# Kernel tuning notes

Measured on AMD Instinct MI355X. Metric: run time of the kernel, lower is better.

The kernel has to match this reference:

```python
import jax, jax.numpy as jnp
import numpy as np
from jax import lax

N_INPUTS = 8
N_OUTPUTS = 4
N_RESERVOIR = 2048
T = 4096
SPECTRAL_RADIUS = 0.95
NOISE = 0.001


def setup_inputs() -> dict:
    key = jax.random.key(0)
    ks = jax.random.split(key, 8)
    inputs = jax.random.normal(ks[0], (T, N_INPUTS), dtype=jnp.float32)
    outputs = jax.random.normal(ks[1], (T, N_OUTPUTS), dtype=jnp.float32)
    # recurrent weights: uniform(-0.5, 0.5), rescaled to spectral radius ~0.95.
    # For a uniform(-0.5,0.5) NxN matrix the spectral radius is ~ sqrt(N/12)
    # (circular law), used here in place of an explicit eigendecomposition.
    w_raw = jax.random.uniform(ks[2], (N_RESERVOIR, N_RESERVOIR), dtype=jnp.float32) - 0.5
    radius = jnp.sqrt(N_RESERVOIR / 12.0)
    w = w_raw * (SPECTRAL_RADIUS / radius)
    w_in = jax.random.uniform(ks[3], (N_RESERVOIR, N_INPUTS), dtype=jnp.float32) * 2.0 - 1.0
    w_feedb = jax.random.uniform(ks[4], (N_RESERVOIR, N_OUTPUTS), dtype=jnp.float32) * 2.0 - 1.0
    # readout (nn.Linear): weight [n_out, R+n_in], bias [n_out]
    fan_in = N_RESERVOIR + N_INPUTS
    bound = 1.0 / np.sqrt(fan_in)
    lin_w = jax.random.uniform(ks[5], (N_OUTPUTS, fan_in), dtype=jnp.float32, minval=-bound, maxval=bound)
    lin_b = jax.random.uniform(ks[6], (N_OUTPUTS,), dtype=jnp.float32, minval=-bound, maxval=bound)
    # per-step regularization noise: noise * (uniform - 0.5), pre-drawn for determinism
    noise_seq = NOISE * (jax.random.uniform(ks[7], (T, N_RESERVOIR), dtype=jnp.float32) - 0.5)
    return {"inputs": inputs, "outputs": outputs, "w": w, "w_in": w_in,
            "w_feedb": w_feedb, "lin_w": lin_w, "lin_b": lin_b, "noise_seq": noise_seq}


def reference(inputs, outputs, w, w_in, w_feedb, lin_w, lin_b, noise_seq):
    # Echo-state recurrence: x_n = tanh(w @ x_{n-1} + w_in @ u_n + w_feedb @ y_{n-1}) + noise_n
    # States row 0 stays zero (original loop starts at n=1).
    R = w.shape[0]

    def step(x, per_step):
        u_n, y_prev, nz = per_step
        x_new = jnp.tanh(w @ x + w_in @ u_n + w_feedb @ y_prev) + nz
        return x_new, x_new

    x0 = jnp.zeros((R,), dtype=inputs.dtype)
    _, xs = lax.scan(step, x0, (inputs[1:], outputs[:-1], noise_seq[1:]))  # [T-1, R]

    zero_row_x = jnp.zeros((1, R), dtype=inputs.dtype)
    zero_row_u = jnp.zeros((1, inputs.shape[1]), dtype=inputs.dtype)
    states_x = jnp.concatenate([zero_row_x, xs], axis=0)              # [T, R]
    states_u = jnp.concatenate([zero_row_u, inputs[1:]], axis=0)       # [T, n_in]
    states = jnp.concatenate([states_x, states_u], axis=1)             # [T, R+n_in]

    out = states @ lin_w.T + lin_b                                     # [T, n_out]
    return out
```

## Files before the change

### kernel.cpp

```cpp
#include <hip/hip_runtime.h>

#define T_STEPS 4096
#define RSIZE   2048
#define N_IN    8
#define N_OUT   4
#define NWG     256
#define NT      256
#define LIN_STRIDE  (RSIZE + N_IN)
#define SENTINEL    0x7FC00000u

typedef float v4 __attribute__((ext_vector_type(4)));


__global__ __launch_bounds__(256) void init_kernel(v4* __restrict__ states4) {
    int idx = blockIdx.x * 256 + threadIdx.x;
    const float s = __uint_as_float(SENTINEL);
    v4 v = (idx < RSIZE / 4) ? (v4){0.f, 0.f, 0.f, 0.f} : (v4){s, s, s, s};
    states4[idx] = v;
}

__device__ __forceinline__ float dot4(v4 a, v4 b) {
    float s = a.x * b.x;
    s = fmaf(a.y, b.y, s);
    s = fmaf(a.z, b.z, s);
    s = fmaf(a.w, b.w, s);
    return s;
}

__global__ __launch_bounds__(NT, 1) void reservoir_kernel(
    const float* __restrict__ W,
    const float* __restrict__ Win,
    const float* __restrict__ Wfb,
    const float* __restrict__ inputs,
    const float* __restrict__ outputs,
    const float* __restrict__ noise,
    float* __restrict__ states)
{
    const int g    = blockIdx.x;
    const int t    = threadIdx.x;
    const int lane = t & 63;
    const int wv   = t >> 6;
    const int wid  = g * 4 + wv;
    const int r0   = wid * 2;

    v4 wreg[2][4][2];
    #pragma unroll
    for (int i = 0; i < 2; ++i)
        #pragma unroll
        for (int j = 0; j < 4; ++j) {
            const float* p = W + (size_t)(r0 + i) * RSIZE + j * 512 + lane * 8;
            wreg[i][j][0] = *(const v4*)p;
            wreg[i][j][1] = *(const v4*)(p + 4);
        }

    float win[N_IN] = {0}, wfb[N_OUT] = {0};
    if (lane < 2) {
        const int r = r0 + lane;
        #pragma unroll
        for (int j = 0; j < N_IN; ++j)  win[j] = Win[r * N_IN + j];
        #pragma unroll
        for (int k = 0; k < N_OUT; ++k) wfb[k] = Wfb[r * N_OUT + k];
    }

    __shared__ v4 xsh[2][RSIZE / 4];
    const int fillc = wv * 512 + lane * 8;
    const int fi    = fillc >> 2;

    for (int n = 1; n < T_STEPS; ++n) {
        float pre = 0.0f, nz = 0.0f;
        if (lane < 2) {
            const int r = r0 + lane;
            nz = noise[(size_t)n * RSIZE + r];
            #pragma unroll
            for (int j = 0; j < N_IN; ++j)  pre = fmaf(win[j], inputs[n * N_IN + j], pre);
            #pragma unroll
            for (int k = 0; k < N_OUT; ++k) pre = fmaf(wfb[k], outputs[(n - 1) * N_OUT + k], pre);
        }

        const volatile v4* src =
            (const volatile v4*)(states + (size_t)(n - 1) * RSIZE + fillc);
        v4 a, b;
        for (;;) {
            a = src[0];
            b = src[1];
            bool ok = (__float_as_uint(a.x) != SENTINEL) &
                      (__float_as_uint(a.y) != SENTINEL) &
                      (__float_as_uint(a.z) != SENTINEL) &
                      (__float_as_uint(a.w) != SENTINEL) &
                      (__float_as_uint(b.x) != SENTINEL) &
                      (__float_as_uint(b.y) != SENTINEL) &
                      (__float_as_uint(b.z) != SENTINEL) &
                      (__float_as_uint(b.w) != SENTINEL);
            if (ok) break;
            __builtin_amdgcn_s_sleep(1);
        }

        const int p = (n - 1) & 1;
        xsh[p][fi]     = a;
        xsh[p][fi + 1] = b;
        __syncthreads();

        float acc0 = 0.0f, acc1 = 0.0f;
        #pragma unroll
        for (int j = 0; j < 4; ++j) {
            const int xi = j * 128 + lane * 2;
            v4 x0 = xsh[p][xi];
            v4 x1 = xsh[p][xi + 1];
            acc0 += dot4(wreg[0][j][0], x0) + dot4(wreg[0][j][1], x1);
            acc1 += dot4(wreg[1][j][0], x0) + dot4(wreg[1][j][1], x1);
        }

        #pragma unroll
        for (int m = 1; m < 64; m <<= 1) {
            acc0 += __shfl_xor(acc0, m, 64);
            acc1 += __shfl_xor(acc1, m, 64);
        }

        if (lane < 2) {
            float s  = (lane == 0 ? acc0 : acc1) + pre;
            float xn = tanhf(s) + nz;
            *(volatile float*)(states + (size_t)n * RSIZE + r0 + lane) = xn;
        }
        __builtin_amdgcn_s_waitcnt(0);
    }
}

__global__ __launch_bounds__(256) void readout_kernel(
    const float* __restrict__ states,
    const float* __restrict__ inputs,
    const float* __restrict__ lin_w,
    const float* __restrict__ lin_b,
    float* __restrict__ out)
{
    const int ti   = blockIdx.x;
    const int tid  = threadIdx.x;
    const int lane = tid & 63;
    const int wave = tid >> 6;
    const int c0   = tid * 8;

    const float* xp = states + (size_t)ti * RSIZE + c0;
    v4 xa = *(const v4*)xp;
    v4 xb = *(const v4*)(xp + 4);

    float acc[N_OUT];
    #pragma unroll
    for (int o = 0; o < N_OUT; ++o) {
        const float* lp = lin_w + (size_t)o * LIN_STRIDE + c0;
        v4 la = *(const v4*)lp;
        v4 lb = *(const v4*)(lp + 4);
        acc[o] = dot4(la, xa) + dot4(lb, xb);
    }

    #pragma unroll
    for (int m = 1; m < 64; m <<= 1) {
        #pragma unroll
        for (int o = 0; o < N_OUT; ++o) acc[o] += __shfl_xor(acc[o], m, 64);
    }

    __shared__ float red[4][N_OUT];
    if (lane == 0) {
        #pragma unroll
        for (int o = 0; o < N_OUT; ++o) red[wave][o] = acc[o];
    }
    __syncthreads();

    if (tid < N_OUT) {
        float s = red[0][tid] + red[1][tid] + red[2][tid] + red[3][tid] + lin_b[tid];
        if (ti > 0) {
            #pragma unroll
            for (int j = 0; j < N_IN; ++j)
                s = fmaf(lin_w[(size_t)tid * LIN_STRIDE + RSIZE + j],
                         inputs[ti * N_IN + j], s);
        }
        out[ti * N_OUT + tid] = s;
    }
}

extern "C" void kernel_launch(void* const* d_in, const int* in_sizes, int n_in,
                              void* d_out, int out_size, void* d_ws, size_t ws_size,
                              hipStream_t stream) {
    const float* inputs  = (const float*)d_in[0];
    const float* outputs = (const float*)d_in[1];
    const float* W       = (const float*)d_in[2];
    const float* Win     = (const float*)d_in[3];
    const float* Wfb     = (const float*)d_in[4];
    const float* lin_w   = (const float*)d_in[5];
    const float* lin_b   = (const float*)d_in[6];
    const float* noise   = (const float*)d_in[7];
    float* out = (float*)d_out;

    float* states = (float*)d_ws;

    hipLaunchKernelGGL(init_kernel, dim3((T_STEPS * RSIZE / 4) / 256), dim3(256), 0,
                       stream, (v4*)states);
    hipLaunchKernelGGL(reservoir_kernel, dim3(NWG), dim3(NT), 0, stream,
                       W, Win, Wfb, inputs, outputs, noise, states);
    hipLaunchKernelGGL(readout_kernel, dim3(T_STEPS), dim3(256), 0, stream,
                       states, inputs, lin_w, lin_b, out);
}
```

Measured before the change: 7.594 ms.

## Halve workgroups to 128 with four rows per wave and transposed reduction

Each wave now computes four reservoir rows instead of two, so only 128 workgroups take part in the per-step global spin-wait handoff. Weights are held in registers with a coalesced layout of one v4 per lane per chunk. The cross-lane reduction uses a butterfly transpose that sums four accumulators with fewer shuffles. Polling is now wave-uniform through __any. Fewer workgroups cut global synchronization and polling traffic per step, at the cost of more register pressure and more FMA work per wave.

```diff
diff --git a/kernel.cpp b/kernel.cpp
--- a/kernel.cpp
+++ b/kernel.cpp
@@ -4,7 +4,7 @@
 #define RSIZE   2048
 #define N_IN    8
 #define N_OUT   4
-#define NWG     256
+#define NWG     128
 #define NT      256
 #define LIN_STRIDE  (RSIZE + N_IN)
 #define SENTINEL    0x7FC00000u
@@ -41,20 +41,17 @@
     const int lane = t & 63;
     const int wv   = t >> 6;
     const int wid  = g * 4 + wv;
-    const int r0   = wid * 2;
-
-    v4 wreg[2][4][2];
+    const int r0   = wid * 4;
+
+    v4 wreg[4][8];
     #pragma unroll
-    for (int i = 0; i < 2; ++i)
-        #pragma unroll
-        for (int j = 0; j < 4; ++j) {
-            const float* p = W + (size_t)(r0 + i) * RSIZE + j * 512 + lane * 8;
-            wreg[i][j][0] = *(const v4*)p;
-            wreg[i][j][1] = *(const v4*)(p + 4);
-        }
+    for (int i = 0; i < 4; ++i)
+        #pragma unroll
+        for (int c = 0; c < 8; ++c)
+            wreg[i][c] = *(const v4*)(W + (size_t)(r0 + i) * RSIZE + c * 256 + lane * 4);
 
     float win[N_IN] = {0}, wfb[N_OUT] = {0};
-    if (lane < 2) {
+    if (lane < 4) {
         const int r = r0 + lane;
         #pragma unroll
         for (int j = 0; j < N_IN; ++j)  win[j] = Win[r * N_IN + j];
@@ -63,12 +60,12 @@
     }
 
     __shared__ v4 xsh[2][RSIZE / 4];
-    const int fillc = wv * 512 + lane * 8;
-    const int fi    = fillc >> 2;
+    const int fi0 = wv * 128 + lane;
+    const int fi1 = wv * 128 + 64 + lane;
 
     for (int n = 1; n < T_STEPS; ++n) {
         float pre = 0.0f, nz = 0.0f;
-        if (lane < 2) {
+        if (lane < 4) {
             const int r = r0 + lane;
             nz = noise[(size_t)n * RSIZE + r];
             #pragma unroll
@@ -77,48 +74,58 @@
             for (int k = 0; k < N_OUT; ++k) pre = fmaf(wfb[k], outputs[(n - 1) * N_OUT + k], pre);
         }
 
-        const volatile v4* src =
-            (const volatile v4*)(states + (size_t)(n - 1) * RSIZE + fillc);
-        v4 a, b;
+        const volatile v4* src0 =
+            (const volatile v4*)(states + (size_t)(n - 1) * RSIZE) + fi0;
+        const volatile v4* src1 =
+            (const volatile v4*)(states + (size_t)(n - 1) * RSIZE) + fi1;
+        v4 a = {0.f, 0.f, 0.f, 0.f}, b = {0.f, 0.f, 0.f, 0.f};
+        bool done = false;
         for (;;) {
-            a = src[0];
-            b = src[1];
-            bool ok = (__float_as_uint(a.x) != SENTINEL) &
-                      (__float_as_uint(a.y) != SENTINEL) &
-                      (__float_as_uint(a.z) != SENTINEL) &
-                      (__float_as_uint(a.w) != SENTINEL) &
-                      (__float_as_uint(b.x) != SENTINEL) &
-                      (__float_as_uint(b.y) != SENTINEL) &
-                      (__float_as_uint(b.z) != SENTINEL) &
-                      (__float_as_uint(b.w) != SENTINEL);
-            if (ok) break;
+            if (!done) {
+                a = *src0;
+                b = *src1;
+                done = (__float_as_uint(a.x) != SENTINEL) &
+                       (__float_as_uint(a.y) != SENTINEL) &
+                       (__float_as_uint(a.z) != SENTINEL) &
+                       (__float_as_uint(a.w) != SENTINEL) &
+                       (__float_as_uint(b.x) != SENTINEL) &
+                       (__float_as_uint(b.y) != SENTINEL) &
+                       (__float_as_uint(b.z) != SENTINEL) &
+                       (__float_as_uint(b.w) != SENTINEL);
+            }
+            if (!__any(!done)) break;
             __builtin_amdgcn_s_sleep(1);
         }
 
         const int p = (n - 1) & 1;
-        xsh[p][fi]     = a;
-        xsh[p][fi + 1] = b;
+        xsh[p][fi0] = a;
+        xsh[p][fi1] = b;
         __syncthreads();
 
-        float acc0 = 0.0f, acc1 = 0.0f;
-        #pragma unroll
-        for (int j = 0; j < 4; ++j) {
-            const int xi = j * 128 + lane * 2;
-            v4 x0 = xsh[p][xi];
-            v4 x1 = xsh[p][xi + 1];
-            acc0 += dot4(wreg[0][j][0], x0) + dot4(wreg[0][j][1], x1);
-            acc1 += dot4(wreg[1][j][0], x0) + dot4(wreg[1][j][1], x1);
-        }
-
-        #pragma unroll
-        for (int m = 1; m < 64; m <<= 1) {
-            acc0 += __shfl_xor(acc0, m, 64);
-            acc1 += __shfl_xor(acc1, m, 64);
-        }
-
-        if (lane < 2) {
-            float s  = (lane == 0 ? acc0 : acc1) + pre;
-            float xn = tanhf(s) + nz;
+        float acc[4] = {0.f, 0.f, 0.f, 0.f};
+        #pragma unroll
+        for (int c = 0; c < 8; ++c) {
+            v4 x = xsh[p][c * 64 + lane];
+            #pragma unroll
+            for (int i = 0; i < 4; ++i) acc[i] = fmaf(1.0f, dot4(wreg[i][c], x), acc[i]);
+        }
+
+        float a0 = (lane & 1) ? acc[1] : acc[0];
+        float s0 = (lane & 1) ? acc[0] : acc[1];
+        float a1 = (lane & 1) ? acc[3] : acc[2];
+        float s1 = (lane & 1) ? acc[2] : acc[3];
+        a0 += __shfl_xor(s0, 1, 64);
+        a1 += __shfl_xor(s1, 1, 64);
+        float b0 = (lane & 2) ? a1 : a0;
+        float sb = (lane & 2) ? a0 : a1;
+        b0 += __shfl_xor(sb, 2, 64);
+        b0 += __shfl_xor(b0, 4, 64);
+        b0 += __shfl_xor(b0, 8, 64);
+        b0 += __shfl_xor(b0, 16, 64);
+        b0 += __shfl_xor(b0, 32, 64);
+
+        if (lane < 4) {
+            float xn = tanhf(b0 + pre) + nz;
             *(volatile float*)(states + (size_t)n * RSIZE + r0 + lane) = xn;
         }
         __builtin_amdgcn_s_waitcnt(0);
```

After: 8.176 ms. 1.08x slower.

## Prefetch next-step inputs, coalesce state polling, and merge dual-row shuffle reduction

Applied to the files above, without the earlier changes.

Precomputes the input and feedback pre-activation and noise for step n+1 while step n runs, so those global loads leave the critical path. State polling now uses contiguous per-lane v4 loads with a wave-wide __all exit, and the W register layout is changed to match. The two row accumulators are folded into a single butterfly reduction, which roughly halves the shuffle count. The trailing s_waitcnt(0) is removed, which could change when the volatile store becomes visible to other workgroups.

```diff
diff --git a/kernel.cpp b/kernel.cpp
--- a/kernel.cpp
+++ b/kernel.cpp
@@ -43,15 +43,12 @@
     const int wid  = g * 4 + wv;
     const int r0   = wid * 2;
 
-    v4 wreg[2][4][2];
+    v4 wreg[2][8];
     #pragma unroll
     for (int i = 0; i < 2; ++i)
         #pragma unroll
-        for (int j = 0; j < 4; ++j) {
-            const float* p = W + (size_t)(r0 + i) * RSIZE + j * 512 + lane * 8;
-            wreg[i][j][0] = *(const v4*)p;
-            wreg[i][j][1] = *(const v4*)(p + 4);
-        }
+        for (int c = 0; c < 8; ++c)
+            wreg[i][c] = *(const v4*)(W + (size_t)(r0 + i) * RSIZE + c * 256 + lane * 4);
 
     float win[N_IN] = {0}, wfb[N_OUT] = {0};
     if (lane < 2) {
@@ -63,65 +60,101 @@
     }
 
     __shared__ v4 xsh[2][RSIZE / 4];
-    const int fillc = wv * 512 + lane * 8;
-    const int fi    = fillc >> 2;
+    const int fi0 = wv * 128 + lane;
+    const int fi1 = wv * 128 + 64 + lane;
+
+    float cur_pre = 0.0f, cur_nz = 0.0f;
+    if (lane < 2) {
+        const int r = r0 + lane;
+        cur_nz = noise[(size_t)RSIZE + r];
+        v4 i0 = *(const v4*)(inputs + N_IN);
+        v4 i1 = *(const v4*)(inputs + N_IN + 4);
+        v4 o0 = *(const v4*)(outputs);
+        float p = 0.0f;
+        p = fmaf(win[0], i0.x, p); p = fmaf(win[1], i0.y, p);
+        p = fmaf(win[2], i0.z, p); p = fmaf(win[3], i0.w, p);
+        p = fmaf(win[4], i1.x, p); p = fmaf(win[5], i1.y, p);
+        p = fmaf(win[6], i1.z, p); p = fmaf(win[7], i1.w, p);
+        p = fmaf(wfb[0], o0.x, p); p = fmaf(wfb[1], o0.y, p);
+        p = fmaf(wfb[2], o0.z, p); p = fmaf(wfb[3], o0.w, p);
+        cur_pre = p;
+    }
 
     for (int n = 1; n < T_STEPS; ++n) {
-        float pre = 0.0f, nz = 0.0f;
+        const volatile v4* base =
+            (const volatile v4*)(states + (size_t)(n - 1) * RSIZE);
+        v4 a = {0.f, 0.f, 0.f, 0.f}, b = {0.f, 0.f, 0.f, 0.f};
+        bool done = false;
+        for (;;) {
+            if (!done) {
+                a = base[fi0];
+                b = base[fi1];
+                done = (__float_as_uint(a.x) != SENTINEL) &
+                       (__float_as_uint(a.y) != SENTINEL) &
+                       (__float_as_uint(a.z) != SENTINEL) &
+                       (__float_as_uint(a.w) != SENTINEL) &
+                       (__float_as_uint(b.x) != SENTINEL) &
+                       (__float_as_uint(b.y) != SENTINEL) &
+                       (__float_as_uint(b.z) != SENTINEL) &
+                       (__float_as_uint(b.w) != SENTINEL);
+            }
+            if (__all(done)) break;
+            __builtin_amdgcn_s_sleep(1);
+        }
+
+        const bool hn = (n + 1 < T_STEPS);
+        v4 ni0 = {0.f,0.f,0.f,0.f}, ni1 = {0.f,0.f,0.f,0.f}, no0 = {0.f,0.f,0.f,0.f};
+        float nnz = 0.0f;
+        if (lane < 2 && hn) {
+            ni0 = *(const v4*)(inputs + (size_t)(n + 1) * N_IN);
+            ni1 = *(const v4*)(inputs + (size_t)(n + 1) * N_IN + 4);
+            no0 = *(const v4*)(outputs + (size_t)n * N_OUT);
+            nnz = noise[(size_t)(n + 1) * RSIZE + r0 + lane];
+        }
+
+        const int p = (n - 1) & 1;
+        xsh[p][fi0] = a;
+        xsh[p][fi1] = b;
+        __syncthreads();
+
+        float a0 = 0.f, a1 = 0.f, b0 = 0.f, b1 = 0.f;
+        #pragma unroll
+        for (int c = 0; c < 4; ++c) {
+            v4 x0 = xsh[p][c * 64 + lane];
+            v4 x1 = xsh[p][(c + 4) * 64 + lane];
+            a0 += dot4(wreg[0][c], x0);
+            b0 += dot4(wreg[0][c + 4], x1);
+            a1 += dot4(wreg[1][c], x0);
+            b1 += dot4(wreg[1][c + 4], x1);
+        }
+        float acc0 = a0 + b0;
+        float acc1 = a1 + b1;
+
+        float mine  = (lane & 1) ? acc1 : acc0;
+        float other = (lane & 1) ? acc0 : acc1;
+        mine += __shfl_xor(other, 1, 64);
+        mine += __shfl_xor(mine, 2, 64);
+        mine += __shfl_xor(mine, 4, 64);
+        mine += __shfl_xor(mine, 8, 64);
+        mine += __shfl_xor(mine, 16, 64);
+        mine += __shfl_xor(mine, 32, 64);
+
         if (lane < 2) {
-            const int r = r0 + lane;
-            nz = noise[(size_t)n * RSIZE + r];
-            #pragma unroll
-            for (int j = 0; j < N_IN; ++j)  pre = fmaf(win[j], inputs[n * N_IN + j], pre);
-            #pragma unroll
-            for (int k = 0; k < N_OUT; ++k) pre = fmaf(wfb[k], outputs[(n - 1) * N_OUT + k], pre);
-        }
-
-        const volatile v4* src =
-            (const volatile v4*)(states + (size_t)(n - 1) * RSIZE + fillc);
-        v4 a, b;
-        for (;;) {
-            a = src[0];
-            b = src[1];
-            bool ok = (__float_as_uint(a.x) != SENTINEL) &
-                      (__float_as_uint(a.y) != SENTINEL) &
-                      (__float_as_uint(a.z) != SENTINEL) &
-                      (__float_as_uint(a.w) != SENTINEL) &
-                      (__float_as_uint(b.x) != SENTINEL) &
-                      (__float_as_uint(b.y) != SENTINEL) &
-                      (__float_as_uint(b.z) != SENTINEL) &
-                      (__float_as_uint(b.w) != SENTINEL);
-            if (ok) break;
-            __builtin_amdgcn_s_sleep(1);
-        }
-
-        const int p = (n - 1) & 1;
-        xsh[p][fi]     = a;
-        xsh[p][fi + 1] = b;
-        __syncthreads();
-
-        float acc0 = 0.0f, acc1 = 0.0f;
-        #pragma unroll
-        for (int j = 0; j < 4; ++j) {
-            const int xi = j * 128 + lane * 2;
-            v4 x0 = xsh[p][xi];
-            v4 x1 = xsh[p][xi + 1];
-            acc0 += dot4(wreg[0][j][0], x0) + dot4(wreg[0][j][1], x1);
-            acc1 += dot4(wreg[1][j][0], x0) + dot4(wreg[1][j][1], x1);
-        }
-
-        #pragma unroll
-        for (int m = 1; m < 64; m <<= 1) {
-            acc0 += __shfl_xor(acc0, m, 64);
-            acc1 += __shfl_xor(acc1, m, 64);
-        }
-
-        if (lane < 2) {
-            float s  = (lane == 0 ? acc0 : acc1) + pre;
-            float xn = tanhf(s) + nz;
+            float xn = tanhf(mine + cur_pre) + cur_nz;
             *(volatile float*)(states + (size_t)n * RSIZE + r0 + lane) = xn;
         }
-        __builtin_amdgcn_s_waitcnt(0);
+
+        if (lane < 2 && hn) {
+            float pnext = 0.0f;
+            pnext = fmaf(win[0], ni0.x, pnext); pnext = fmaf(win[1], ni0.y, pnext);
+            pnext = fmaf(win[2], ni0.z, pnext); pnext = fmaf(win[3], ni0.w, pnext);
+            pnext = fmaf(win[4], ni1.x, pnext); pnext = fmaf(win[5], ni1.y, pnext);
+            pnext = fmaf(win[6], ni1.z, pnext); pnext = fmaf(win[7], ni1.w, pnext);
+            pnext = fmaf(wfb[0], no0.x, pnext); pnext = fmaf(wfb[1], no0.y, pnext);
+            pnext = fmaf(wfb[2], no0.z, pnext); pnext = fmaf(wfb[3], no0.w, pnext);
+            cur_pre = pnext;
+            cur_nz  = nnz;
+        }
     }
 }
 
```

Measured after the change: 11.27 ms. 48.4% more time.
